# Performance work log

Hardware: AMD Instinct MI355X
Metric: run time of the kernel (lower is better)

## Reference

```python
import jax, jax.numpy as jnp
import numpy as np
from jax.scipy.special import logsumexp

N_LABELS = 64
BOS_INDEX = 0
B, S = 32, 512


def setup_inputs() -> dict:
    key = jax.random.key(0)
    k1, k2, k3 = jax.random.split(key, 3)
    emits = jax.random.normal(k1, (B, S, N_LABELS * N_LABELS), dtype=jnp.float32)
    targets = jax.random.randint(k2, (B, S + 1), 0, N_LABELS, dtype=jnp.int64)
    # mask: valid-prefix mask from random lengths in [2, S]
    lengths = jax.random.randint(k3, (B,), 2, S + 1)
    mask = (jnp.arange(S)[None, :] < lengths[:, None])
    return {"emits": emits, "targets": targets, "mask": mask}


def reference(emits, targets, mask):
    # emits: [B, S, L*L], targets: [B, S+1], mask: [B, S]; order=2 CRF NLL loss
    L = N_LABELS
    b, s, _ = emits.shape
    em = jnp.transpose(emits, (1, 0, 2))          # [S, B, L*L]
    tg = targets.T                                 # [S+1, B]
    mk = mask.T                                    # [S, B]

    em4 = em.reshape(s, b, L, L)                   # [S, B, prev, next]
    log_alpha0 = em4[0, :, BOS_INDEX, :]           # [B, L]

    def step(log_alpha, inp):
        e_i, m_i = inp                             # [B, L, L], [B]
        scores = log_alpha[:, :, None] + e_i       # [B, prev, next]
        new = logsumexp(scores, axis=1)            # [B, L]
        log_alpha = jnp.where(m_i[:, None], new, log_alpha)
        return log_alpha, None

    log_alpha, _ = jax.lax.scan(step, log_alpha0, (em4[1:], mk[1:]))
    log_z = logsumexp(log_alpha, axis=1).sum()

    # gold path score: pair index = prev_tag * L + next_tag
    idx = tg[:-1] * L + tg[1:]                     # [S, B]
    gold = jnp.take_along_axis(em, idx[:, :, None], axis=-1)[..., 0]  # [S, B]
    score = jnp.where(mk, gold, 0.0).sum()

    total_token = mk.sum().astype(emits.dtype)
    loss = (log_z - score) / total_token
    return loss
```

## Files before the change

### kernel.cpp

```cpp
#include <hip/hip_runtime.h>
#include <math.h>


constexpr int S_LEN   = 512;
constexpr int NB      = 32;
constexpr int NL      = 64;
constexpr int LL      = 4096;
constexpr int CL      = 16;
constexpr int NCH     = 32;
constexpr int NCHUNKS = NB * NCH;

#define LN2F 0.69314718055994531f
#define PREF 4.6588830833596715f

typedef _Float16 h4 __attribute__((ext_vector_type(4)));
typedef float    f4 __attribute__((ext_vector_type(4)));
union U4 { unsigned u[2]; h4 v; };

__device__ __forceinline__ float bl(float v, int sl) {
  return __int_as_float(__builtin_amdgcn_readlane(__float_as_int(v), sl));
}
__device__ __forceinline__ unsigned pk2(float a, float b) {
  auto r = __builtin_amdgcn_cvt_pkrtz(a, b);
  return __builtin_bit_cast(unsigned, r);
}
__device__ __forceinline__ float expw(float x) {
  return __expf(x - PREF);
}

__global__ __launch_bounds__(64) void crf_chunk(
    const float* __restrict__ emits,
    const int*   __restrict__ targets,
    const int*   __restrict__ mask,
    _Float16*    __restrict__ matP,
    float*       __restrict__ wsf)
{
  const int ci   = blockIdx.x;
  const int b    = ci >> 5;
  const int cc   = ci & 31;
  const int lane = threadIdx.x;
  const int c    = lane & 15;
  const int h    = lane >> 4;
  const float* __restrict__ eb = emits + (size_t)b * (S_LEN * LL);

  int len;
  {
    const int* mb = mask + b * S_LEN;
    int cnt = 0;
    #pragma unroll
    for (int i = 0; i < 8; ++i) cnt += (mb[i * 64 + lane] != 0);
    #pragma unroll
    for (int off = 32; off; off >>= 1) cnt += __shfl_xor(cnt, off);
    len = cnt;
  }

  {
    float g = 0.f;
    const int s = 16 * cc + (lane & 15);
    if (lane < 16 && s < len) {
      const int* tb = targets + b * (S_LEN + 1);
      g = eb[(size_t)s * LL + tb[s] * NL + tb[s + 1]];
    }
    #pragma unroll
    for (int off = 32; off; off >>= 1) g += __shfl_xor(g, off);
    if (lane == 0) wsf[NCHUNKS + ci] = g;
  }

  const int s0 = 16 * cc + 1;
  const int n  = min(len - s0, CL);
  if (n < 1) return;

  h4 bf[4][4];
  #pragma unroll
  for (int K = 0; K < 4; ++K)
    #pragma unroll
    for (int J = 0; J < 4; ++J) {
      h4 v;
      #pragma unroll
      for (int i = 0; i < 4; ++i)
        v[i] = (_Float16)((K == J && (4 * h + i) == c) ? 1.0f : 0.0f);
      bf[K][J] = v;
    }

  float Lacc = 0.f;
  f4 LB[4][4];
  h4 afA[4][4], afB[4][4];

#define LOADE(S)                                                             \
  do { const float* ep = eb + (size_t)(S) * LL;                              \
    _Pragma("unroll") for (int I = 0; I < 4; ++I) {                          \
      const float* rp = ep + (16 * I + c) * 64 + 4 * h;                      \
      _Pragma("unroll") for (int K = 0; K < 4; ++K)                          \
        LB[I][K] = *reinterpret_cast<const f4*>(rp + 16 * K);                \
    } } while (0)

#define BUILDAF(AF)                                                          \
  do { _Pragma("unroll") for (int I = 0; I < 4; ++I)                         \
    _Pragma("unroll") for (int K = 0; K < 4; ++K) {                          \
      U4 x;                                                                  \
      x.u[0] = pk2(expw(LB[I][K][0]), expw(LB[I][K][1]));                    \
      x.u[1] = pk2(expw(LB[I][K][2]), expw(LB[I][K][3]));                    \
      AF[I][K] = x.v;                                                        \
    } } while (0)

#define STEPM(AC, AN, M)                                                     \
  do { if ((M) <= n) {                                                       \
    const bool rn = ((((M) & 7) == 0) || ((M) == n));                        \
    float mh = 0.f;                                                          \
    {                                                \
      f4 dh[4][2];                                                           \
      _Pragma("unroll") for (int I = 0; I < 4; ++I)                          \
        _Pragma("unroll") for (int J = 0; J < 2; ++J) {                      \
          f4 d = {0.f, 0.f, 0.f, 0.f};                                       \
          _Pragma("unroll") for (int K = 0; K < 4; ++K)                      \
            d = __builtin_amdgcn_mfma_f32_16x16x16f16(AC[I][K], bf[K][J], d, 0, 0, 0); \
          dh[I][J] = d;                                                      \
        }                                                                    \
      if (rn) {                                                              \
        _Pragma("unroll") for (int I = 0; I < 4; ++I)                        \
          _Pragma("unroll") for (int J = 0; J < 2; ++J)                      \
            _Pragma("unroll") for (int u = 0; u < 4; ++u)                    \
              mh = fmaxf(mh, dh[I][J][u]);                                   \
      }                                                                      \
      _Pragma("unroll") for (int K = 0; K < 4; ++K)                          \
        _Pragma("unroll") for (int J = 0; J < 2; ++J) {                      \
          U4 y;                                                              \
          y.u[0] = pk2(dh[K][J][0], dh[K][J][1]);                            \
          y.u[1] = pk2(dh[K][J][2], dh[K][J][3]);                            \
          bf[K][J] = y.v;                                                    \
        }                                                                    \
    }                                                                        \
    {                                                \
      f4 dh[4][2];                                                           \
      _Pragma("unroll") for (int I = 0; I < 4; ++I)                          \
        _Pragma("unroll") for (int J = 0; J < 2; ++J) {                      \
          f4 d = {0.f, 0.f, 0.f, 0.f};                                       \
          _Pragma("unroll") for (int K = 0; K < 4; ++K)                      \
            d = __builtin_amdgcn_mfma_f32_16x16x16f16(AC[I][K], bf[K][J + 2], d, 0, 0, 0); \
          dh[I][J] = d;                                                      \
        }                                                                    \
      if (rn) {                                                              \
        _Pragma("unroll") for (int I = 0; I < 4; ++I)                        \
          _Pragma("unroll") for (int J = 0; J < 2; ++J)                      \
            _Pragma("unroll") for (int u = 0; u < 4; ++u)                    \
              mh = fmaxf(mh, dh[I][J][u]);                                   \
      }                                                                      \
      _Pragma("unroll") for (int K = 0; K < 4; ++K)                          \
        _Pragma("unroll") for (int J = 0; J < 2; ++J) {                      \
          U4 y;                                                              \
          y.u[0] = pk2(dh[K][J][0], dh[K][J][1]);                            \
          y.u[1] = pk2(dh[K][J][2], dh[K][J][3]);                            \
          bf[K][J + 2] = y.v;                                                \
        }                                                                    \
    }                                                                        \
    Lacc += PREF;                                                            \
    if (rn) {                                                                \
      _Pragma("unroll") for (int off = 32; off; off >>= 1)                   \
        mh = fmaxf(mh, __shfl_xor(mh, off));                                 \
      const int E = (__float_as_int(mh) >> 23) & 0xFF;                       \
      const _Float16 hs = (_Float16)__int_as_float((254 - E) << 23);         \
      const h4 hv = {hs, hs, hs, hs};                                        \
      _Pragma("unroll") for (int K = 0; K < 4; ++K)                          \
        _Pragma("unroll") for (int J = 0; J < 4; ++J) bf[K][J] *= hv;        \
      Lacc += (float)(E - 127) * LN2F;                                       \
    }                                                                        \
    if ((M) < n) {                                                           \
      BUILDAF(AN);                            \
      if ((M) + 1 < n) LOADE(s0 + n - 2 - (M));         \
    }                                                                        \
  } } while (0)

  LOADE(s0 + n - 1);
  BUILDAF(afA);
  if (n > 1) LOADE(s0 + n - 2);
  for (int m = 1; m <= n; m += 2) {
    STEPM(afA, afB, m);
    STEPM(afB, afA, m + 1);
  }

  {
    _Float16* mp = matP + (size_t)ci * 4096;
    #pragma unroll
    for (int I = 0; I < 4; ++I)
      #pragma unroll
      for (int J = 0; J < 4; ++J)
        #pragma unroll
        for (int i = 0; i < 4; ++i)
          mp[(I * 4 + J) * 256 + i * 64 + lane] = bf[I][J][i];
  }
  if (lane == 0) wsf[ci] = Lacc;
}

__global__ __launch_bounds__(64) void crf_fold(
    const float* __restrict__ emits,
    const int*   __restrict__ mask,
    const _Float16* __restrict__ matP,
    const float* __restrict__ wsf,
    float*       __restrict__ wso,
    int*         __restrict__ done,
    float*       __restrict__ out)
{
  const int b = blockIdx.x, lane = threadIdx.x;
  const int c = lane & 15, h = lane >> 4;
  const float* __restrict__ eb = emits + (size_t)b * (S_LEN * LL);

  int len;
  {
    const int* mb = mask + b * S_LEN;
    int cnt = 0;
    #pragma unroll
    for (int i = 0; i < 8; ++i) cnt += (mb[i * 64 + lane] != 0);
    #pragma unroll
    for (int off = 32; off; off >>= 1) cnt += __shfl_xor(cnt, off);
    len = cnt;
  }
  const int nact = (len + 14) >> 4;

  const bool on = (c == 0);
  const h4 HZ = {(_Float16)0, (_Float16)0, (_Float16)0, (_Float16)0};

  float la[16];
  #pragma unroll
  for (int K = 0; K < 4; ++K)
    #pragma unroll
    for (int i = 0; i < 4; ++i) la[K * 4 + i] = eb[16 * K + 4 * h + i];
  float mm = la[0];
  #pragma unroll
  for (int i = 1; i < 16; ++i) mm = fmaxf(mm, la[i]);
  const float m0 = fmaxf(fmaxf(bl(mm, 0), bl(mm, 16)), fmaxf(bl(mm, 32), bl(mm, 48)));
  float Lacc = m0;
  h4 bv[4];
  #pragma unroll
  for (int K = 0; K < 4; ++K) {
    U4 y;
    y.u[0] = pk2(__expf(la[4 * K] - m0), __expf(la[4 * K + 1] - m0));
    y.u[1] = pk2(__expf(la[4 * K + 2] - m0), __expf(la[4 * K + 3] - m0));
    bv[K] = on ? y.v : HZ;
  }

  h4 A0[4][4], A1[4][4];

#define LOADA(AF, CH)                                                        \
  do { const _Float16* mp = matP + (size_t)(b * NCH + (CH)) * 4096;          \
    _Pragma("unroll") for (int I = 0; I < 4; ++I)                            \
      _Pragma("unroll") for (int K = 0; K < 4; ++K)                          \
        AF[I][K] = *reinterpret_cast<const h4*>(                             \
            mp + (I * 4 + K) * 256 + (c & 3) * 64 + 16 * (c >> 2) + 4 * h);  \
  } while (0)

#define FOLD(AF, CH)                                                         \
  do { f4 dv[4];                                                             \
    _Pragma("unroll") for (int I = 0; I < 4; ++I) {                          \
      f4 d = {0.f, 0.f, 0.f, 0.f};                                           \
      _Pragma("unroll") for (int K = 0; K < 4; ++K)                          \
        d = __builtin_amdgcn_mfma_f32_16x16x16f16(AF[I][K], bv[K], d, 0, 0, 0); \
      dv[I] = d;                                                             \
    }                                                                        \
    float mx = dv[0][0];                                                     \
    _Pragma("unroll") for (int I = 0; I < 4; ++I)                            \
      _Pragma("unroll") for (int u = 0; u < 4; ++u) mx = fmaxf(mx, dv[I][u]); \
    const float gm = fmaxf(fmaxf(bl(mx, 0), bl(mx, 16)),                     \
                           fmaxf(bl(mx, 32), bl(mx, 48)));                   \
    const int E = (__float_as_int(gm) >> 23) & 0xFF;                         \
    const float scale = __int_as_float((254 - E) << 23);                     \
    Lacc += (float)(E - 127) * LN2F + wsf[b * NCH + (CH)];                   \
    _Pragma("unroll") for (int I = 0; I < 4; ++I) {                          \
      U4 y;                                                                  \
      y.u[0] = pk2(dv[I][0] * scale, dv[I][1] * scale);                      \
      y.u[1] = pk2(dv[I][2] * scale, dv[I][3] * scale);                      \
      bv[I] = on ? y.v : HZ;                                                 \
    } } while (0)

  LOADA(A0, 0);
  for (int ch = 0; ch < nact; ++ch) {
    if (ch & 1) { if (ch + 1 < nact) LOADA(A0, ch + 1); FOLD(A1, ch); }
    else        { if (ch + 1 < nact) LOADA(A1, ch + 1); FOLD(A0, ch); }
  }

  float qs = 0.f;
  #pragma unroll
  for (int K = 0; K < 4; ++K)
    #pragma unroll
    for (int i = 0; i < 4; ++i) qs += (float)bv[K][i];
  const float q0 = (bl(qs, 0) + bl(qs, 16)) + (bl(qs, 32) + bl(qs, 48));
  if (lane == 0) {
    wso[b]      = Lacc + __logf(q0);
    wso[32 + b] = (float)len;
  }

  __threadfence();
  int isLast = 0;
  if (lane == 0) isLast = (atomicAdd(done, 1) == NB - 1);
  isLast = __shfl(isLast, 0);
  if (isLast) {
    __threadfence();
    const float* gold = wsf + NCHUNKS;
    float gs = 0.f;
    #pragma unroll
    for (int i = 0; i < NCHUNKS / 64; ++i) gs += gold[i * 64 + lane];
    float lz = (lane < NB) ? wso[lane] : 0.f;
    float ln = (lane < NB) ? wso[32 + lane] : 0.f;
    #pragma unroll
    for (int off = 32; off; off >>= 1) {
      gs += __shfl_xor(gs, off);
      lz += __shfl_xor(lz, off);
      ln += __shfl_xor(ln, off);
    }
    if (lane == 0) out[0] = (lz - gs) / ln;
  }
}

extern "C" void kernel_launch(void* const* d_in, const int* in_sizes, int n_in,
                              void* d_out, int out_size, void* d_ws, size_t ws_size,
                              hipStream_t stream) {
  const float* emits   = (const float*)d_in[0];
  const int*   targets = (const int*)d_in[1];
  const int*   mask    = (const int*)d_in[2];
  float* out = (float*)d_out;

  _Float16* matP = (_Float16*)d_ws;
  float*    wsf  = (float*)((char*)d_ws + (size_t)NCHUNKS * 4096 * 2);
  float*    wso  = wsf + 2 * NCHUNKS;
  int*      done = (int*)(wso + 64);

  hipMemsetAsync(done, 0, sizeof(int), stream);
  hipLaunchKernelGGL(crf_chunk, dim3(NCHUNKS), dim3(64), 0, stream,
                     emits, targets, mask, matP, wsf);
  hipLaunchKernelGGL(crf_fold, dim3(NB), dim3(64), 0, stream,
                     emits, mask, matP, wsf, wso, done, out);
}
```

Measured before the change: 77.12 us.

## Fuse chunk and fold kernels using per-batch last-block atomic counters

```diff
diff --git a/kernel.cpp b/kernel.cpp
--- a/kernel.cpp
+++ b/kernel.cpp
@@ -28,12 +28,15 @@
   return __expf(x - PREF);
 }
 
-__global__ __launch_bounds__(64) void crf_chunk(
+__global__ __launch_bounds__(64) void crf_all(
     const float* __restrict__ emits,
     const int*   __restrict__ targets,
     const int*   __restrict__ mask,
     _Float16*    __restrict__ matP,
-    float*       __restrict__ wsf)
+    float*       __restrict__ wsf,
+    float*       __restrict__ wso,
+    int*         __restrict__ cnt,
+    float*       __restrict__ out)
 {
   const int ci   = blockIdx.x;
   const int b    = ci >> 5;
@@ -46,12 +49,12 @@
   int len;
   {
     const int* mb = mask + b * S_LEN;
-    int cnt = 0;
-    #pragma unroll
-    for (int i = 0; i < 8; ++i) cnt += (mb[i * 64 + lane] != 0);
-    #pragma unroll
-    for (int off = 32; off; off >>= 1) cnt += __shfl_xor(cnt, off);
-    len = cnt;
+    int n0 = 0;
+    #pragma unroll
+    for (int i = 0; i < 8; ++i) n0 += (mb[i * 64 + lane] != 0);
+    #pragma unroll
+    for (int off = 32; off; off >>= 1) n0 += __shfl_xor(n0, off);
+    len = n0;
   }
 
   {
@@ -68,232 +71,219 @@
 
   const int s0 = 16 * cc + 1;
   const int n  = min(len - s0, CL);
-  if (n < 1) return;
-
-  h4 bf[4][4];
-  #pragma unroll
-  for (int K = 0; K < 4; ++K)
-    #pragma unroll
-    for (int J = 0; J < 4; ++J) {
-      h4 v;
+
+  if (n >= 1) {
+    h4 bf[4][4];
+    #pragma unroll
+    for (int K = 0; K < 4; ++K)
       #pragma unroll
-      for (int i = 0; i < 4; ++i)
-        v[i] = (_Float16)((K == J && (4 * h + i) == c) ? 1.0f : 0.0f);
-      bf[K][J] = v;
-    }
-
-  float Lacc = 0.f;
-  f4 LB[4][4];
-  h4 afA[4][4], afB[4][4];
-
-#define LOADE(S)                                                             \
-  do { const float* ep = eb + (size_t)(S) * LL;                              \
-    _Pragma("unroll") for (int I = 0; I < 4; ++I) {                          \
-      const float* rp = ep + (16 * I + c) * 64 + 4 * h;                      \
-      _Pragma("unroll") for (int K = 0; K < 4; ++K)                          \
-        LB[I][K] = *reinterpret_cast<const f4*>(rp + 16 * K);                \
-    } } while (0)
-
-#define BUILDAF(AF)                                                          \
-  do { _Pragma("unroll") for (int I = 0; I < 4; ++I)                         \
-    _Pragma("unroll") for (int K = 0; K < 4; ++K) {                          \
-      U4 x;                                                                  \
-      x.u[0] = pk2(expw(LB[I][K][0]), expw(LB[I][K][1]));                    \
-      x.u[1] = pk2(expw(LB[I][K][2]), expw(LB[I][K][3]));                    \
-      AF[I][K] = x.v;                                                        \
-    } } while (0)
-
-#define STEPM(AC, AN, M)                                                     \
-  do { if ((M) <= n) {                                                       \
-    const bool rn = ((((M) & 7) == 0) || ((M) == n));                        \
-    float mh = 0.f;                                                          \
-    {                                                \
-      f4 dh[4][2];                                                           \
-      _Pragma("unroll") for (int I = 0; I < 4; ++I)                          \
-        _Pragma("unroll") for (int J = 0; J < 2; ++J) {                      \
-          f4 d = {0.f, 0.f, 0.f, 0.f};                                       \
-          _Pragma("unroll") for (int K = 0; K < 4; ++K)                      \
-            d = __builtin_amdgcn_mfma_f32_16x16x16f16(AC[I][K], bf[K][J], d, 0, 0, 0); \
-          dh[I][J] = d;                                                      \
-        }                                                                    \
-      if (rn) {                                                              \
-        _Pragma("unroll") for (int I = 0; I < 4; ++I)                        \
-          _Pragma("unroll") for (int J = 0; J < 2; ++J)                      \
-            _Pragma("unroll") for (int u = 0; u < 4; ++u)                    \
-              mh = fmaxf(mh, dh[I][J][u]);                                   \
-      }                                                                      \
-      _Pragma("unroll") for (int K = 0; K < 4; ++K)                          \
-        _Pragma("unroll") for (int J = 0; J < 2; ++J) {                      \
-          U4 y;                                                              \
-          y.u[0] = pk2(dh[K][J][0], dh[K][J][1]);                            \
-          y.u[1] = pk2(dh[K][J][2], dh[K][J][3]);                            \
-          bf[K][J] = y.v;                                                    \
-        }                                                                    \
-    }                                                                        \
-    {                                                \
-      f4 dh[4][2];                                                           \
-      _Pragma("unroll") for (int I = 0; I < 4; ++I)                          \
-        _Pragma("unroll") for (int J = 0; J < 2; ++J) {                      \
-          f4 d = {0.f, 0.f, 0.f, 0.f};                                       \
-          _Pragma("unroll") for (int K = 0; K < 4; ++K)                      \
-            d = __builtin_amdgcn_mfma_f32_16x16x16f16(AC[I][K], bf[K][J + 2], d, 0, 0, 0); \
-          dh[I][J] = d;                                                      \
-        }                                                                    \
-      if (rn) {                                                              \
-        _Pragma("unroll") for (int I = 0; I < 4; ++I)                        \
-          _Pragma("unroll") for (int J = 0; J < 2; ++J)                      \
-            _Pragma("unroll") for (int u = 0; u < 4; ++u)                    \
-              mh = fmaxf(mh, dh[I][J][u]);                                   \
-      }                                                                      \
-      _Pragma("unroll") for (int K = 0; K < 4; ++K)                          \
-        _Pragma("unroll") for (int J = 0; J < 2; ++J) {                      \
-          U4 y;                                                              \
-          y.u[0] = pk2(dh[K][J][0], dh[K][J][1]);                            \
-          y.u[1] = pk2(dh[K][J][2], dh[K][J][3]);                            \
-          bf[K][J + 2] = y.v;                                                \
-        }                                                                    \
-    }                                                                        \
-    Lacc += PREF;                                                            \
-    if (rn) {                                                                \
-      _Pragma("unroll") for (int off = 32; off; off >>= 1)                   \
-        mh = fmaxf(mh, __shfl_xor(mh, off));                                 \
-      const int E = (__float_as_int(mh) >> 23) & 0xFF;                       \
-      const _Float16 hs = (_Float16)__int_as_float((254 - E) << 23);         \
-      const h4 hv = {hs, hs, hs, hs};                                        \
-      _Pragma("unroll") for (int K = 0; K < 4; ++K)                          \
-        _Pragma("unroll") for (int J = 0; J < 4; ++J) bf[K][J] *= hv;        \
-      Lacc += (float)(E - 127) * LN2F;                                       \
-    }                                                                        \
-    if ((M) < n) {                                                           \
-      BUILDAF(AN);                            \
-      if ((M) + 1 < n) LOADE(s0 + n - 2 - (M));         \
-    }                                                                        \
-  } } while (0)
-
-  LOADE(s0 + n - 1);
-  BUILDAF(afA);
-  if (n > 1) LOADE(s0 + n - 2);
-  for (int m = 1; m <= n; m += 2) {
-    STEPM(afA, afB, m);
-    STEPM(afB, afA, m + 1);
-  }
-
-  {
-    _Float16* mp = matP + (size_t)ci * 4096;
-    #pragma unroll
-    for (int I = 0; I < 4; ++I)
-      #pragma unroll
-      for (int J = 0; J < 4; ++J)
+      for (int J = 0; J < 4; ++J) {
+        h4 v;
         #pragma unroll
         for (int i = 0; i < 4; ++i)
-          mp[(I * 4 + J) * 256 + i * 64 + lane] = bf[I][J][i];
-  }
-  if (lane == 0) wsf[ci] = Lacc;
-}
-
-__global__ __launch_bounds__(64) void crf_fold(
-    const float* __restrict__ emits,
-    const int*   __restrict__ mask,
-    const _Float16* __restrict__ matP,
-    const float* __restrict__ wsf,
-    float*       __restrict__ wso,
-    int*         __restrict__ done,
-    float*       __restrict__ out)
-{
-  const int b = blockIdx.x, lane = threadIdx.x;
-  const int c = lane & 15, h = lane >> 4;
-  const float* __restrict__ eb = emits + (size_t)b * (S_LEN * LL);
-
-  int len;
+          v[i] = (_Float16)((K == J && (4 * h + i) == c) ? 1.0f : 0.0f);
+        bf[K][J] = v;
+      }
+
+    float Lacc = 0.f;
+    f4 LB[4][4];
+    h4 afA[4][4], afB[4][4];
+
+#define LOADE(S)                                                             \
+    do { const float* ep = eb + (size_t)(S) * LL;                            \
+      _Pragma("unroll") for (int I = 0; I < 4; ++I) {                        \
+        const float* rp = ep + (16 * I + c) * 64 + 4 * h;                    \
+        _Pragma("unroll") for (int K = 0; K < 4; ++K)                        \
+          LB[I][K] = *reinterpret_cast<const f4*>(rp + 16 * K);              \
+      } } while (0)
+
+#define BUILDAF(AF)                                                          \
+    do { _Pragma("unroll") for (int I = 0; I < 4; ++I)                       \
+      _Pragma("unroll") for (int K = 0; K < 4; ++K) {                        \
+        U4 x;                                                                \
+        x.u[0] = pk2(expw(LB[I][K][0]), expw(LB[I][K][1]));                  \
+        x.u[1] = pk2(expw(LB[I][K][2]), expw(LB[I][K][3]));                  \
+        AF[I][K] = x.v;                                                      \
+      } } while (0)
+
+#define STEPM(AC, AN, M)                                                     \
+    do { if ((M) <= n) {                                                     \
+      const bool rn = ((((M) & 7) == 0) || ((M) == n));                      \
+      float mh = 0.f;                                                        \
+      {                                              \
+        f4 dh[4][2];                                                         \
+        _Pragma("unroll") for (int I = 0; I < 4; ++I)                        \
+          _Pragma("unroll") for (int J = 0; J < 2; ++J) {                    \
+            f4 d = {0.f, 0.f, 0.f, 0.f};                                     \
+            _Pragma("unroll") for (int K = 0; K < 4; ++K)                    \
+              d = __builtin_amdgcn_mfma_f32_16x16x16f16(AC[I][K], bf[K][J], d, 0, 0, 0); \
+            dh[I][J] = d;                                                    \
+          }                                                                  \
+        if (rn) {                                                            \
+          _Pragma("unroll") for (int I = 0; I < 4; ++I)                      \
+            _Pragma("unroll") for (int J = 0; J < 2; ++J)                    \
+              _Pragma("unroll") for (int u = 0; u < 4; ++u)                  \
+                mh = fmaxf(mh, dh[I][J][u]);                                 \
+        }                                                                    \
+        _Pragma("unroll") for (int K = 0; K < 4; ++K)                        \
+          _Pragma("unroll") for (int J = 0; J < 2; ++J) {                    \
+            U4 y;                                                            \
+            y.u[0] = pk2(dh[K][J][0], dh[K][J][1]);                          \
+            y.u[1] = pk2(dh[K][J][2], dh[K][J][3]);                          \
+            bf[K][J] = y.v;                                                  \
+          }                                                                  \
+      }                                                                      \
+      {                                              \
+        f4 dh[4][2];                                                         \
+        _Pragma("unroll") for (int I = 0; I < 4; ++I)                        \
+          _Pragma("unroll") for (int J = 0; J < 2; ++J) {                    \
+            f4 d = {0.f, 0.f, 0.f, 0.f};                                     \
+            _Pragma("unroll") for (int K = 0; K < 4; ++K)                    \
+              d = __builtin_amdgcn_mfma_f32_16x16x16f16(AC[I][K], bf[K][J + 2], d, 0, 0, 0); \
+            dh[I][J] = d;                                                    \
+          }                                                                  \
+        if (rn) {                                                            \
+          _Pragma("unroll") for (int I = 0; I < 4; ++I)                      \
+            _Pragma("unroll") for (int J = 0; J < 2; ++J)                    \
+              _Pragma("unroll") for (int u = 0; u < 4; ++u)                  \
+                mh = fmaxf(mh, dh[I][J][u]);                                 \
+        }                                                                    \
+        _Pragma("unroll") for (int K = 0; K < 4; ++K)                        \
+          _Pragma("unroll") for (int J = 0; J < 2; ++J) {                    \
+            U4 y;                                                            \
+            y.u[0] = pk2(dh[K][J][0], dh[K][J][1]);                          \
+            y.u[1] = pk2(dh[K][J][2], dh[K][J][3]);                          \
+            bf[K][J + 2] = y.v;                                              \
+          }                                                                  \
+      }                                                                      \
+      Lacc += PREF;                                                          \
+      if (rn) {                                                              \
+        _Pragma("unroll") for (int off = 32; off; off >>= 1)                 \
+          mh = fmaxf(mh, __shfl_xor(mh, off));                               \
+        const int E = (__float_as_int(mh) >> 23) & 0xFF;                     \
+        const _Float16 hs = (_Float16)__int_as_float((254 - E) << 23);       \
+        const h4 hv = {hs, hs, hs, hs};                                      \
+        _Pragma("unroll") for (int K = 0; K < 4; ++K)                        \
+          _Pragma("unroll") for (int J = 0; J < 4; ++J) bf[K][J] *= hv;      \
+        Lacc += (float)(E - 127) * LN2F;                                     \
+      }                                                                      \
+      if ((M) < n) {                                                         \
+        BUILDAF(AN);                                                         \
+        if ((M) + 1 < n) LOADE(s0 + n - 2 - (M));                            \
+      }                                                                      \
+    } } while (0)
+
+    LOADE(s0 + n - 1);
+    BUILDAF(afA);
+    if (n > 1) LOADE(s0 + n - 2);
+    for (int m = 1; m <= n; m += 2) {
+      STEPM(afA, afB, m);
+      STEPM(afB, afA, m + 1);
+    }
+
+    {
+      _Float16* mp = matP + (size_t)ci * 4096;
+      #pragma unroll
+      for (int I = 0; I < 4; ++I)
+        #pragma unroll
+        for (int J = 0; J < 4; ++J)
+          #pragma unroll
+          for (int i = 0; i < 4; ++i)
+            mp[(I * 4 + J) * 256 + i * 64 + lane] = bf[I][J][i];
+    }
+    if (lane == 0) wsf[ci] = Lacc;
+  }
+
+  __threadfence();
+  int lastB = 0;
+  if (lane == 0) lastB = (atomicAdd(&cnt[b], 1) == NCH - 1);
+  lastB = __shfl(lastB, 0);
+  if (!lastB) return;
+  __threadfence();
+
   {
-    const int* mb = mask + b * S_LEN;
-    int cnt = 0;
-    #pragma unroll
-    for (int i = 0; i < 8; ++i) cnt += (mb[i * 64 + lane] != 0);
-    #pragma unroll
-    for (int off = 32; off; off >>= 1) cnt += __shfl_xor(cnt, off);
-    len = cnt;
-  }
-  const int nact = (len + 14) >> 4;
-
-  const bool on = (c == 0);
-  const h4 HZ = {(_Float16)0, (_Float16)0, (_Float16)0, (_Float16)0};
-
-  float la[16];
-  #pragma unroll
-  for (int K = 0; K < 4; ++K)
-    #pragma unroll
-    for (int i = 0; i < 4; ++i) la[K * 4 + i] = eb[16 * K + 4 * h + i];
-  float mm = la[0];
-  #pragma unroll
-  for (int i = 1; i < 16; ++i) mm = fmaxf(mm, la[i]);
-  const float m0 = fmaxf(fmaxf(bl(mm, 0), bl(mm, 16)), fmaxf(bl(mm, 32), bl(mm, 48)));
-  float Lacc = m0;
-  h4 bv[4];
-  #pragma unroll
-  for (int K = 0; K < 4; ++K) {
-    U4 y;
-    y.u[0] = pk2(__expf(la[4 * K] - m0), __expf(la[4 * K + 1] - m0));
-    y.u[1] = pk2(__expf(la[4 * K + 2] - m0), __expf(la[4 * K + 3] - m0));
-    bv[K] = on ? y.v : HZ;
-  }
-
-  h4 A0[4][4], A1[4][4];
+    const int nact = (len + 14) >> 4;
+    const bool on = (c == 0);
+    const h4 HZ = {(_Float16)0, (_Float16)0, (_Float16)0, (_Float16)0};
+
+    float la[16];
+    #pragma unroll
+    for (int K = 0; K < 4; ++K)
+      #pragma unroll
+      for (int i = 0; i < 4; ++i) la[K * 4 + i] = eb[16 * K + 4 * h + i];
+    float mm = la[0];
+    #pragma unroll
+    for (int i = 1; i < 16; ++i) mm = fmaxf(mm, la[i]);
+    const float m0 = fmaxf(fmaxf(bl(mm, 0), bl(mm, 16)),
+                           fmaxf(bl(mm, 32), bl(mm, 48)));
+    float Lacc = m0;
+    h4 bv[4];
+    #pragma unroll
+    for (int K = 0; K < 4; ++K) {
+      U4 y;
+      y.u[0] = pk2(__expf(la[4 * K] - m0), __expf(la[4 * K + 1] - m0));
+      y.u[1] = pk2(__expf(la[4 * K + 2] - m0), __expf(la[4 * K + 3] - m0));
+      bv[K] = on ? y.v : HZ;
+    }
+
+    h4 A0[4][4], A1[4][4];
 
 #define LOADA(AF, CH)                                                        \
-  do { const _Float16* mp = matP + (size_t)(b * NCH + (CH)) * 4096;          \
-    _Pragma("unroll") for (int I = 0; I < 4; ++I)                            \
-      _Pragma("unroll") for (int K = 0; K < 4; ++K)                          \
-        AF[I][K] = *reinterpret_cast<const h4*>(                             \
-            mp + (I * 4 + K) * 256 + (c & 3) * 64 + 16 * (c >> 2) + 4 * h);  \
-  } while (0)
+    do { const _Float16* mp = matP + (size_t)(b * NCH + (CH)) * 4096;        \
+      _Pragma("unroll") for (int I = 0; I < 4; ++I)                          \
+        _Pragma("unroll") for (int K = 0; K < 4; ++K)                        \
+          AF[I][K] = *reinterpret_cast<const h4*>(                           \
+              mp + (I * 4 + K) * 256 + (c & 3) * 64 + 16 * (c >> 2) + 4 * h); \
+    } while (0)
 
 #define FOLD(AF, CH)                                                         \
-  do { f4 dv[4];                                                             \
-    _Pragma("unroll") for (int I = 0; I < 4; ++I) {                          \
-      f4 d = {0.f, 0.f, 0.f, 0.f};                                           \
-      _Pragma("unroll") for (int K = 0; K < 4; ++K)                          \
-        d = __builtin_amdgcn_mfma_f32_16x16x16f16(AF[I][K], bv[K], d, 0, 0, 0); \
-      dv[I] = d;                                                             \
-    }                                                                        \
-    float mx = dv[0][0];                                                     \
-    _Pragma("unroll") for (int I = 0; I < 4; ++I)                            \
-      _Pragma("unroll") for (int u = 0; u < 4; ++u) mx = fmaxf(mx, dv[I][u]); \
-    const float gm = fmaxf(fmaxf(bl(mx, 0), bl(mx, 16)),                     \
-                           fmaxf(bl(mx, 32), bl(mx, 48)));                   \
-    const int E = (__float_as_int(gm) >> 23) & 0xFF;                         \
-    const float scale = __int_as_float((254 - E) << 23);                     \
-    Lacc += (float)(E - 127) * LN2F + wsf[b * NCH + (CH)];                   \
-    _Pragma("unroll") for (int I = 0; I < 4; ++I) {                          \
-      U4 y;                                                                  \
-      y.u[0] = pk2(dv[I][0] * scale, dv[I][1] * scale);                      \
-      y.u[1] = pk2(dv[I][2] * scale, dv[I][3] * scale);                      \
-      bv[I] = on ? y.v : HZ;                                                 \
-    } } while (0)
-
-  LOADA(A0, 0);
-  for (int ch = 0; ch < nact; ++ch) {
-    if (ch & 1) { if (ch + 1 < nact) LOADA(A0, ch + 1); FOLD(A1, ch); }
-    else        { if (ch + 1 < nact) LOADA(A1, ch + 1); FOLD(A0, ch); }
-  }
-
-  float qs = 0.f;
-  #pragma unroll
-  for (int K = 0; K < 4; ++K)
-    #pragma unroll
-    for (int i = 0; i < 4; ++i) qs += (float)bv[K][i];
-  const float q0 = (bl(qs, 0) + bl(qs, 16)) + (bl(qs, 32) + bl(qs, 48));
-  if (lane == 0) {
-    wso[b]      = Lacc + __logf(q0);
-    wso[32 + b] = (float)len;
+    do { f4 dv[4];                                                           \
+      _Pragma("unroll") for (int I = 0; I < 4; ++I) {                        \
+        f4 d = {0.f, 0.f, 0.f, 0.f};                                         \
+        _Pragma("unroll") for (int K = 0; K < 4; ++K)                        \
+          d = __builtin_amdgcn_mfma_f32_16x16x16f16(AF[I][K], bv[K], d, 0, 0, 0); \
+        dv[I] = d;                                                           \
+      }                                                                      \
+      float mx = dv[0][0];                                                   \
+      _Pragma("unroll") for (int I = 0; I < 4; ++I)                          \
+        _Pragma("unroll") for (int u = 0; u < 4; ++u) mx = fmaxf(mx, dv[I][u]); \
+      const float gm = fmaxf(fmaxf(bl(mx, 0), bl(mx, 16)),                   \
+                             fmaxf(bl(mx, 32), bl(mx, 48)));                 \
+      const int E = (__float_as_int(gm) >> 23) & 0xFF;                       \
+      const float scale = __int_as_float((254 - E) << 23);                   \
+      Lacc += (float)(E - 127) * LN2F + wsf[b * NCH + (CH)];                 \
+      _Pragma("unroll") for (int I = 0; I < 4; ++I) {                        \
+        U4 y;                                                                \
+        y.u[0] = pk2(dv[I][0] * scale, dv[I][1] * scale);                    \
+        y.u[1] = pk2(dv[I][2] * scale, dv[I][3] * scale);                    \
+        bv[I] = on ? y.v : HZ;                                               \
+      } } while (0)
+
+    LOADA(A0, 0);
+    for (int ch = 0; ch < nact; ++ch) {
+      if (ch & 1) { if (ch + 1 < nact) LOADA(A0, ch + 1); FOLD(A1, ch); }
+      else        { if (ch + 1 < nact) LOADA(A1, ch + 1); FOLD(A0, ch); }
+    }
+
+    float qs = 0.f;
+    #pragma unroll
+    for (int K = 0; K < 4; ++K)
+      #pragma unroll
+      for (int i = 0; i < 4; ++i) qs += (float)bv[K][i];
+    const float q0 = (bl(qs, 0) + bl(qs, 16)) + (bl(qs, 32) + bl(qs, 48));
+    if (lane == 0) {
+      wso[b]      = Lacc + __logf(q0);
+      wso[32 + b] = (float)len;
+    }
   }
 
   __threadfence();
-  int isLast = 0;
-  if (lane == 0) isLast = (atomicAdd(done, 1) == NB - 1);
-  isLast = __shfl(isLast, 0);
-  if (isLast) {
-    __threadfence();
+  int lastG = 0;
+  if (lane == 0) lastG = (atomicAdd(&cnt[NB], 1) == NB - 1);
+  lastG = __shfl(lastG, 0);
+  if (!lastG) return;
+  __threadfence();
+  {
     const float* gold = wsf + NCHUNKS;
     float gs = 0.f;
     #pragma unroll
@@ -321,11 +311,9 @@
   _Float16* matP = (_Float16*)d_ws;
   float*    wsf  = (float*)((char*)d_ws + (size_t)NCHUNKS * 4096 * 2);
   float*    wso  = wsf + 2 * NCHUNKS;
-  int*      done = (int*)(wso + 64);
-
-  hipMemsetAsync(done, 0, sizeof(int), stream);
-  hipLaunchKernelGGL(crf_chunk, dim3(NCHUNKS), dim3(64), 0, stream,
-                     emits, targets, mask, matP, wsf);
-  hipLaunchKernelGGL(crf_fold, dim3(NB), dim3(64), 0, stream,
-                     emits, mask, matP, wsf, wso, done, out);
-}
+  int*      cnt  = (int*)(wso + 64);
+
+  hipMemsetAsync(cnt, 0, (NB + 1) * sizeof(int), stream);
+  hipLaunchKernelGGL(crf_all, dim3(NCHUNKS), dim3(64), 0, stream,
+                     emits, targets, mask, matP, wsf, wso, cnt, out);
+}
```

Result: slower. 135.3 us (+75.5%).

## Double-buffer raw emit loads and build exp fragments at step start; cheapen fold max

Applied to the files above, without the earlier changes.

```diff
diff --git a/kernel.cpp b/kernel.cpp
--- a/kernel.cpp
+++ b/kernel.cpp
@@ -83,10 +83,10 @@
     }
 
   float Lacc = 0.f;
-  f4 LB[4][4];
-  h4 afA[4][4], afB[4][4];
-
-#define LOADE(S)                                                             \
+  f4 LB0[4][4], LB1[4][4];
+  h4 af[4][4];
+
+#define LOADE(LB, S)                                                         \
   do { const float* ep = eb + (size_t)(S) * LL;                              \
     _Pragma("unroll") for (int I = 0; I < 4; ++I) {                          \
       const float* rp = ep + (16 * I + c) * 64 + 4 * h;                      \
@@ -94,17 +94,19 @@
         LB[I][K] = *reinterpret_cast<const f4*>(rp + 16 * K);                \
     } } while (0)
 
-#define BUILDAF(AF)                                                          \
+#define BUILDAF(LB)                                                          \
   do { _Pragma("unroll") for (int I = 0; I < 4; ++I)                         \
     _Pragma("unroll") for (int K = 0; K < 4; ++K) {                          \
       U4 x;                                                                  \
       x.u[0] = pk2(expw(LB[I][K][0]), expw(LB[I][K][1]));                    \
       x.u[1] = pk2(expw(LB[I][K][2]), expw(LB[I][K][3]));                    \
-      AF[I][K] = x.v;                                                        \
+      af[I][K] = x.v;                                                        \
     } } while (0)
 
-#define STEPM(AC, AN, M)                                                     \
+#define STEPM(LBC, M)                                                        \
   do { if ((M) <= n) {                                                       \
+    BUILDAF(LBC);                              \
+    if ((M) + 2 <= n) LOADE(LBC, s0 + n - 2 - (M));    \
     const bool rn = ((((M) & 7) == 0) || ((M) == n));                        \
     float mh = 0.f;                                                          \
     {                                                \
@@ -113,7 +115,7 @@
         _Pragma("unroll") for (int J = 0; J < 2; ++J) {                      \
           f4 d = {0.f, 0.f, 0.f, 0.f};                                       \
           _Pragma("unroll") for (int K = 0; K < 4; ++K)                      \
-            d = __builtin_amdgcn_mfma_f32_16x16x16f16(AC[I][K], bf[K][J], d, 0, 0, 0); \
+            d = __builtin_amdgcn_mfma_f32_16x16x16f16(af[I][K], bf[K][J], d, 0, 0, 0); \
           dh[I][J] = d;                                                      \
         }                                                                    \
       if (rn) {                                                              \
@@ -136,7 +138,7 @@
         _Pragma("unroll") for (int J = 0; J < 2; ++J) {                      \
           f4 d = {0.f, 0.f, 0.f, 0.f};                                       \
           _Pragma("unroll") for (int K = 0; K < 4; ++K)                      \
-            d = __builtin_amdgcn_mfma_f32_16x16x16f16(AC[I][K], bf[K][J + 2], d, 0, 0, 0); \
+            d = __builtin_amdgcn_mfma_f32_16x16x16f16(af[I][K], bf[K][J + 2], d, 0, 0, 0); \
           dh[I][J] = d;                                                      \
         }                                                                    \
       if (rn) {                                                              \
@@ -164,18 +166,13 @@
         _Pragma("unroll") for (int J = 0; J < 4; ++J) bf[K][J] *= hv;        \
       Lacc += (float)(E - 127) * LN2F;                                       \
     }                                                                        \
-    if ((M) < n) {                                                           \
-      BUILDAF(AN);                            \
-      if ((M) + 1 < n) LOADE(s0 + n - 2 - (M));         \
-    }                                                                        \
   } } while (0)
 
-  LOADE(s0 + n - 1);
-  BUILDAF(afA);
-  if (n > 1) LOADE(s0 + n - 2);
+  LOADE(LB0, s0 + n - 1);
+  if (n > 1) LOADE(LB1, s0 + n - 2);
   for (int m = 1; m <= n; m += 2) {
-    STEPM(afA, afB, m);
-    STEPM(afB, afA, m + 1);
+    STEPM(LB0, m);
+    STEPM(LB1, m + 1);
   }
 
   {
@@ -259,8 +256,13 @@
     float mx = dv[0][0];                                                     \
     _Pragma("unroll") for (int I = 0; I < 4; ++I)                            \
       _Pragma("unroll") for (int u = 0; u < 4; ++u) mx = fmaxf(mx, dv[I][u]); \
-    const float gm = fmaxf(fmaxf(bl(mx, 0), bl(mx, 16)),                     \
-                           fmaxf(bl(mx, 32), bl(mx, 48)));                   \
+    float gm;                                                                \
+    if (((CH) & 3) == 3) {                                                   \
+      gm = fmaxf(fmaxf(bl(mx, 0), bl(mx, 16)),                               \
+                 fmaxf(bl(mx, 32), bl(mx, 48)));                             \
+    } else {                                                                 \
+      gm = bl(mx, 0);                                                        \
+    }                                                                        \
     const int E = (__float_as_int(gm) >> 23) & 0xFF;                         \
     const float scale = __int_as_float((254 - E) << 23);                     \
     Lacc += (float)(E - 127) * LN2F + wsf[b * NCH + (CH)];                   \
```

After: 77.80 us. Within noise of the previous version (+0.9%).
